# Kernel optimization log

Hardware: AMD Instinct MI355X
Metric: run time of the kernel (lower is better)

Reference implementation:

```python
import jax, jax.numpy as jnp
import numpy as np

N_NODES = 100000


def _gcn_conv(x, W, b, src, dst, n_nodes):
    # PyG GCNConv: h = x @ W; add self-loops; symmetric normalization
    # deg over destination (with self-loops), norm = d^-1/2[src] * d^-1/2[dst];
    # out[dst] += norm * h[src]; then + bias.
    h = x @ W  # [N, out_dim]
    loop = jnp.arange(n_nodes, dtype=src.dtype)
    s = jnp.concatenate([src, loop])
    d = jnp.concatenate([dst, loop])
    deg = jax.ops.segment_sum(jnp.ones_like(s, dtype=h.dtype), d, num_segments=n_nodes)
    dinv = jnp.where(deg > 0, jax.lax.rsqrt(deg), 0.0)
    norm = dinv[s] * dinv[d]  # [E+N]
    msg = h[s] * norm[:, None]  # gather + scale
    out = jax.ops.segment_sum(msg, d, num_segments=n_nodes)
    return out + b


def setup_inputs() -> dict:
    key = jax.random.key(0)
    k1, k2, k3, k4 = jax.random.split(key, 4)
    n, f, h, e = N_NODES, 128, 16, 3200000
    x = jax.random.normal(k1, (n, f), dtype=jnp.float32)
    edge_index = jax.random.randint(k2, (2, e), 0, n, dtype=jnp.int64)
    W1 = jax.random.normal(k3, (f, h), dtype=jnp.float32) * (1.0 / np.sqrt(f))
    b1 = jnp.zeros((h,), dtype=jnp.float32)
    W2 = jax.random.normal(k4, (h, h), dtype=jnp.float32) * (1.0 / np.sqrt(h))
    b2 = jnp.zeros((h,), dtype=jnp.float32)
    return {"x": x, "edge_index": edge_index, "W1": W1, "b1": b1, "W2": W2, "b2": b2}


def reference(x, edge_index, W1, b1, W2, b2):
    src, dst = edge_index[0], edge_index[1]
    h = _gcn_conv(x, W1, b1, src, dst, N_NODES)
    h = jax.nn.relu(h)
    out = _gcn_conv(h, W2, b2, src, dst, N_NODES)
    return out
```

## Files before the change

### kernel.cpp

```cpp
#include <hip/hip_runtime.h>

#define N_NODES 100000
#define F_IN 128
#define HD 16
#define NBKT 782
#define NPB 128
#define CHUNK 32768

__global__ __launch_bounds__(256) void k_bcnt(const int* __restrict__ dst, int* __restrict__ wgcnt,
                                              int E, int nwg) {
    __shared__ int hist[NBKT];
    const int t = threadIdx.x, wg = blockIdx.x;
    for (int b = t; b < NBKT; b += 256) hist[b] = 0;
    __syncthreads();
    const int e0 = wg * CHUNK;
    for (int it = 0; it < CHUNK / 1024; ++it) {
        int idx = e0 + it * 1024 + t * 4;
        if (idx + 3 < E) {
            int4 d = *(const int4*)(dst + idx);
            atomicAdd(&hist[d.x >> 7], 1);
            atomicAdd(&hist[d.y >> 7], 1);
            atomicAdd(&hist[d.z >> 7], 1);
            atomicAdd(&hist[d.w >> 7], 1);
        } else {
            int lim = min(idx + 4, E);
            for (int e = idx; e < lim; ++e) atomicAdd(&hist[dst[e] >> 7], 1);
        }
    }
    __syncthreads();
    for (int b = t; b < NBKT; b += 256) wgcnt[b * nwg + wg] = hist[b];
}

__global__ __launch_bounds__(128) void k_btot(const int* __restrict__ wgcnt, int* __restrict__ tot, int nwg) {
    __shared__ int s[128];
    const int b = blockIdx.x, t = threadIdx.x;
    s[t] = (t < nwg) ? wgcnt[b * nwg + t] : 0;
    __syncthreads();
    for (int off = 64; off > 0; off >>= 1) { if (t < off) s[t] += s[t + off]; __syncthreads(); }
    if (t == 0) tot[b] = s[0];
}

__global__ __launch_bounds__(1024) void k_escan(const int* __restrict__ tot, int* __restrict__ ebase) {
    __shared__ int s[1024];
    const int t = threadIdx.x;
    int v = (t < NBKT) ? tot[t] : 0;
    s[t] = v; __syncthreads();
    for (int off = 1; off < 1024; off <<= 1) {
        int x = (t >= off) ? s[t - off] : 0;
        __syncthreads();
        s[t] += x;
        __syncthreads();
    }
    if (t < NBKT) ebase[t] = s[t] - v;
    if (t == NBKT - 1) ebase[NBKT] = s[t];
}

__global__ __launch_bounds__(128) void k_bscan(const int* __restrict__ wgcnt, const int* __restrict__ ebase,
                                               int* __restrict__ base, int nwg) {
    __shared__ int s[128];
    const int b = blockIdx.x, t = threadIdx.x;
    int v = (t < nwg) ? wgcnt[b * nwg + t] : 0;
    s[t] = v; __syncthreads();
    for (int off = 1; off < 128; off <<= 1) {
        int x = (t >= off) ? s[t - off] : 0;
        __syncthreads();
        s[t] += x;
        __syncthreads();
    }
    if (t < nwg) base[b * nwg + t] = ebase[b] + s[t] - v;
}

__global__ __launch_bounds__(256) void k_bscatter(const int* __restrict__ src, const int* __restrict__ dst,
                                                  const int* __restrict__ base, unsigned* __restrict__ srt,
                                                  int E, int nwg) {
    __shared__ int cur[NBKT];
    const int t = threadIdx.x, wg = blockIdx.x;
    for (int b = t; b < NBKT; b += 256) cur[b] = base[b * nwg + wg];
    __syncthreads();
    const int e0 = wg * CHUNK;
    for (int it = 0; it < CHUNK / 1024; ++it) {
        int idx = e0 + it * 1024 + t * 4;
        if (idx + 3 < E) {
            int4 s4 = *(const int4*)(src + idx);
            int4 d4 = *(const int4*)(dst + idx);
            int p;
            p = atomicAdd(&cur[d4.x >> 7], 1); srt[p] = ((unsigned)s4.x << 7) | (unsigned)(d4.x & 127);
            p = atomicAdd(&cur[d4.y >> 7], 1); srt[p] = ((unsigned)s4.y << 7) | (unsigned)(d4.y & 127);
            p = atomicAdd(&cur[d4.z >> 7], 1); srt[p] = ((unsigned)s4.z << 7) | (unsigned)(d4.z & 127);
            p = atomicAdd(&cur[d4.w >> 7], 1); srt[p] = ((unsigned)s4.w << 7) | (unsigned)(d4.w & 127);
        } else {
            int lim = min(idx + 4, E);
            for (int e = idx; e < lim; ++e) {
                int p = atomicAdd(&cur[dst[e] >> 7], 1);
                srt[p] = ((unsigned)src[e] << 7) | (unsigned)(dst[e] & 127);
            }
        }
    }
}

__global__ __launch_bounds__(256) void k_bsort(const unsigned* __restrict__ srt,
                                               const int* __restrict__ ebase,
                                               int* __restrict__ srt2,
                                               int* __restrict__ rs,
                                               float* __restrict__ dinv) {
    __shared__ int cnt_s[NPB];
    __shared__ int sc[NPB];
    __shared__ int cur_s[NPB];
    const int t = threadIdx.x, b = blockIdx.x;
    const int beg = ebase[b], end = ebase[b + 1];

    if (t < NPB) cnt_s[t] = 0;
    __syncthreads();
    for (int i = beg + t; i < end; i += 256) atomicAdd(&cnt_s[srt[i] & 127], 1);
    __syncthreads();

    if (t < NPB) sc[t] = cnt_s[t];
    __syncthreads();
    for (int off = 1; off < NPB; off <<= 1) {
        int v = (t < NPB && t >= off) ? sc[t - off] : 0;
        __syncthreads();
        if (t < NPB) sc[t] += v;
        __syncthreads();
    }
    if (t < NPB) {
        int start = beg + sc[t] - cnt_s[t];
        cur_s[t] = start;
        int node = b * NPB + t;
        if (node <= N_NODES) rs[node] = start;
        if (node < N_NODES) dinv[node] = rsqrtf((float)(cnt_s[t] + 1));
    }
    __syncthreads();
    for (int i = beg + t; i < end; i += 256) {
        unsigned p = srt[i];
        int pos = atomicAdd(&cur_s[p & 127], 1);
        srt2[pos] = (int)(p >> 7);
    }
}

__global__ __launch_bounds__(256) void k_h1(
        const float* __restrict__ x, const float* __restrict__ W1,
        const float* __restrict__ dinv, float* __restrict__ hs) {
    __shared__ float ws[F_IN * HD];
    __shared__ float xs[16][F_IN + 1];
    const int t = threadIdx.x;
    const int node0 = blockIdx.x * 16;

    for (int i = t; i < F_IN * HD; i += 256) ws[i] = W1[i];
    for (int i = t; i < 16 * F_IN; i += 256) {
        int r = i >> 7, c = i & 127;
        int n = node0 + r;
        xs[r][c] = (n < N_NODES) ? x[n * F_IN + c] : 0.0f;
    }
    __syncthreads();

    const int row = t >> 4, col = t & 15;
    const int node = node0 + row;
    float acc = 0.0f;
#pragma unroll 8
    for (int k = 0; k < F_IN; ++k)
        acc += xs[row][k] * ws[k * HD + col];

    if (node < N_NODES) hs[node * HD + col] = acc * dinv[node];
}

__global__ __launch_bounds__(256) void k_h2(
        const float* __restrict__ out1, const float* __restrict__ W2,
        const float* __restrict__ dinv, float* __restrict__ hs) {
    __shared__ float ws[HD * HD];
    __shared__ float as[16][HD + 1];
    const int t = threadIdx.x;
    const int node0 = blockIdx.x * 16;

    if (t < HD * HD) ws[t] = W2[t];
    {
        int n = node0 + (t >> 4);
        float v = (n < N_NODES) ? out1[node0 * HD + t] : 0.0f;
        as[t >> 4][t & 15] = fmaxf(v, 0.0f);
    }
    __syncthreads();

    const int row = t >> 4, col = t & 15;
    const int node = node0 + row;
    float acc = 0.0f;
#pragma unroll
    for (int k = 0; k < HD; ++k)
        acc += as[row][k] * ws[k * HD + col];

    if (node < N_NODES) hs[node * HD + col] = acc * dinv[node];
}

__global__ __launch_bounds__(256) void k_agg(
        const int* __restrict__ srt2, const int* __restrict__ rs,
        const float* __restrict__ dinv, const float* __restrict__ hs,
        const float* __restrict__ bias, float* __restrict__ out) {
    const int node = blockIdx.x * 4 + (threadIdx.x >> 6);
    if (node >= N_NODES) return;
    const int lane = threadIdx.x & 63;
    const int slot = lane >> 2;
    const int c4 = lane & 3;

    const int beg = rs[node];
    const int n   = rs[node + 1] - beg;
    const float4* __restrict__ h4 = (const float4*)hs;

    float4 a = make_float4(0.0f, 0.0f, 0.0f, 0.0f);
    for (int i = slot; i < n; i += 16) {
        int s = srt2[beg + i];
        float4 v = h4[s * 4 + c4];
        a.x += v.x; a.y += v.y; a.z += v.z; a.w += v.w;
    }
#pragma unroll
    for (int m = 4; m <= 32; m <<= 1) {
        a.x += __shfl_xor(a.x, m);
        a.y += __shfl_xor(a.y, m);
        a.z += __shfl_xor(a.z, m);
        a.w += __shfl_xor(a.w, m);
    }
    if (slot == 0) {
        float4 hv = h4[node * 4 + c4];
        float4 bb = ((const float4*)bias)[c4];
        float dd = dinv[node];
        float4 o;
        o.x = dd * (a.x + hv.x) + bb.x;
        o.y = dd * (a.y + hv.y) + bb.y;
        o.z = dd * (a.z + hv.z) + bb.z;
        o.w = dd * (a.w + hv.w) + bb.w;
        ((float4*)out)[node * 4 + c4] = o;
    }
}

extern "C" void kernel_launch(void* const* d_in, const int* in_sizes, int n_in,
                              void* d_out, int out_size, void* d_ws, size_t ws_size,
                              hipStream_t stream) {
    const float* x   = (const float*)d_in[0];
    const int*   ei  = (const int*)d_in[1];
    const float* W1  = (const float*)d_in[2];
    const float* b1  = (const float*)d_in[3];
    const float* W2  = (const float*)d_in[4];
    const float* b2  = (const float*)d_in[5];
    float* out = (float*)d_out;

    const int E = in_sizes[1] / 2;
    const int* src = ei;
    const int* dst = ei + E;
    const int nwg = (E + CHUNK - 1) / CHUNK;

    char* wsb = (char*)d_ws;
    int*      wgcnt = (int*)(wsb + 0x0000000);
    int*      base  = (int*)(wsb + 0x0060000);
    int*      tot   = (int*)(wsb + 0x00C0000);
    int*      ebase = (int*)(wsb + 0x00C2000);
    float*    dinv  = (float*)(wsb + 0x00D0000);
    int*      rs    = (int*)(wsb + 0x0140000);
    unsigned* srt   = (unsigned*)(wsb + 0x0200000);
    float*    hs    = (float*)(wsb + 0x0200000);
    float*    out1  = (float*)(wsb + 0x0900000);
    int*      srt2  = (int*)(wsb + 0x1000000);

    const int tileBlocks = (N_NODES + 15) / 16;
    const int aggBlocks  = (N_NODES + 3) / 4;

    k_bcnt<<<nwg, 256, 0, stream>>>(dst, wgcnt, E, nwg);
    k_btot<<<NBKT, 128, 0, stream>>>(wgcnt, tot, nwg);
    k_escan<<<1, 1024, 0, stream>>>(tot, ebase);
    k_bscan<<<NBKT, 128, 0, stream>>>(wgcnt, ebase, base, nwg);
    k_bscatter<<<nwg, 256, 0, stream>>>(src, dst, base, srt, E, nwg);
    k_bsort<<<NBKT, 256, 0, stream>>>(srt, ebase, srt2, rs, dinv);

    k_h1<<<tileBlocks, 256, 0, stream>>>(x, W1, dinv, hs);
    k_agg<<<aggBlocks, 256, 0, stream>>>(srt2, rs, dinv, hs, b1, out1);

    k_h2<<<tileBlocks, 256, 0, stream>>>(out1, W2, dinv, hs);
    k_agg<<<aggBlocks, 256, 0, stream>>>(srt2, rs, dinv, hs, b2, out);
}
```

Measured before the change: 305.7 us.

## Store node features in fp16 for aggregation gathers and shrink sort chunks

```diff
diff --git a/kernel.cpp b/kernel.cpp
--- a/kernel.cpp
+++ b/kernel.cpp
@@ -1,21 +1,25 @@
 #include <hip/hip_runtime.h>
+#include <hip/hip_fp16.h>
 
 #define N_NODES 100000
 #define F_IN 128
 #define HD 16
 #define NBKT 782
 #define NPB 128
-#define CHUNK 32768
-
-__global__ __launch_bounds__(256) void k_bcnt(const int* __restrict__ dst, int* __restrict__ wgcnt,
-                                              int E, int nwg) {
+#define CHUNK 8192
+#define BTHREADS 512
+
+typedef __attribute__((ext_vector_type(4))) _Float16 half4;
+
+__global__ __launch_bounds__(BTHREADS) void k_bcnt(const int* __restrict__ dst, int* __restrict__ wgcnt,
+                                                   int E, int nwg) {
     __shared__ int hist[NBKT];
     const int t = threadIdx.x, wg = blockIdx.x;
-    for (int b = t; b < NBKT; b += 256) hist[b] = 0;
+    for (int b = t; b < NBKT; b += BTHREADS) hist[b] = 0;
     __syncthreads();
     const int e0 = wg * CHUNK;
-    for (int it = 0; it < CHUNK / 1024; ++it) {
-        int idx = e0 + it * 1024 + t * 4;
+    for (int it = 0; it < CHUNK / (BTHREADS * 4); ++it) {
+        int idx = e0 + it * (BTHREADS * 4) + t * 4;
         if (idx + 3 < E) {
             int4 d = *(const int4*)(dst + idx);
             atomicAdd(&hist[d.x >> 7], 1);
@@ -28,15 +32,15 @@
         }
     }
     __syncthreads();
-    for (int b = t; b < NBKT; b += 256) wgcnt[b * nwg + wg] = hist[b];
-}
-
-__global__ __launch_bounds__(128) void k_btot(const int* __restrict__ wgcnt, int* __restrict__ tot, int nwg) {
-    __shared__ int s[128];
+    for (int b = t; b < NBKT; b += BTHREADS) wgcnt[b * nwg + wg] = hist[b];
+}
+
+__global__ __launch_bounds__(512) void k_btot(const int* __restrict__ wgcnt, int* __restrict__ tot, int nwg) {
+    __shared__ int s[512];
     const int b = blockIdx.x, t = threadIdx.x;
     s[t] = (t < nwg) ? wgcnt[b * nwg + t] : 0;
     __syncthreads();
-    for (int off = 64; off > 0; off >>= 1) { if (t < off) s[t] += s[t + off]; __syncthreads(); }
+    for (int off = 256; off > 0; off >>= 1) { if (t < off) s[t] += s[t + off]; __syncthreads(); }
     if (t == 0) tot[b] = s[0];
 }
 
@@ -55,13 +59,13 @@
     if (t == NBKT - 1) ebase[NBKT] = s[t];
 }
 
-__global__ __launch_bounds__(128) void k_bscan(const int* __restrict__ wgcnt, const int* __restrict__ ebase,
+__global__ __launch_bounds__(512) void k_bscan(const int* __restrict__ wgcnt, const int* __restrict__ ebase,
                                                int* __restrict__ base, int nwg) {
-    __shared__ int s[128];
+    __shared__ int s[512];
     const int b = blockIdx.x, t = threadIdx.x;
     int v = (t < nwg) ? wgcnt[b * nwg + t] : 0;
     s[t] = v; __syncthreads();
-    for (int off = 1; off < 128; off <<= 1) {
+    for (int off = 1; off < 512; off <<= 1) {
         int x = (t >= off) ? s[t - off] : 0;
         __syncthreads();
         s[t] += x;
@@ -70,16 +74,16 @@
     if (t < nwg) base[b * nwg + t] = ebase[b] + s[t] - v;
 }
 
-__global__ __launch_bounds__(256) void k_bscatter(const int* __restrict__ src, const int* __restrict__ dst,
-                                                  const int* __restrict__ base, unsigned* __restrict__ srt,
-                                                  int E, int nwg) {
+__global__ __launch_bounds__(BTHREADS) void k_bscatter(const int* __restrict__ src, const int* __restrict__ dst,
+                                                       const int* __restrict__ base, unsigned* __restrict__ srt,
+                                                       int E, int nwg) {
     __shared__ int cur[NBKT];
     const int t = threadIdx.x, wg = blockIdx.x;
-    for (int b = t; b < NBKT; b += 256) cur[b] = base[b * nwg + wg];
+    for (int b = t; b < NBKT; b += BTHREADS) cur[b] = base[b * nwg + wg];
     __syncthreads();
     const int e0 = wg * CHUNK;
-    for (int it = 0; it < CHUNK / 1024; ++it) {
-        int idx = e0 + it * 1024 + t * 4;
+    for (int it = 0; it < CHUNK / (BTHREADS * 4); ++it) {
+        int idx = e0 + it * (BTHREADS * 4) + t * 4;
         if (idx + 3 < E) {
             int4 s4 = *(const int4*)(src + idx);
             int4 d4 = *(const int4*)(dst + idx);
@@ -139,7 +143,7 @@
 
 __global__ __launch_bounds__(256) void k_h1(
         const float* __restrict__ x, const float* __restrict__ W1,
-        const float* __restrict__ dinv, float* __restrict__ hs) {
+        const float* __restrict__ dinv, _Float16* __restrict__ hs) {
     __shared__ float ws[F_IN * HD];
     __shared__ float xs[16][F_IN + 1];
     const int t = threadIdx.x;
@@ -160,12 +164,12 @@
     for (int k = 0; k < F_IN; ++k)
         acc += xs[row][k] * ws[k * HD + col];
 
-    if (node < N_NODES) hs[node * HD + col] = acc * dinv[node];
+    if (node < N_NODES) hs[node * HD + col] = (_Float16)(acc * dinv[node]);
 }
 
 __global__ __launch_bounds__(256) void k_h2(
         const float* __restrict__ out1, const float* __restrict__ W2,
-        const float* __restrict__ dinv, float* __restrict__ hs) {
+        const float* __restrict__ dinv, _Float16* __restrict__ hs) {
     __shared__ float ws[HD * HD];
     __shared__ float as[16][HD + 1];
     const int t = threadIdx.x;
@@ -186,12 +190,12 @@
     for (int k = 0; k < HD; ++k)
         acc += as[row][k] * ws[k * HD + col];
 
-    if (node < N_NODES) hs[node * HD + col] = acc * dinv[node];
+    if (node < N_NODES) hs[node * HD + col] = (_Float16)(acc * dinv[node]);
 }
 
 __global__ __launch_bounds__(256) void k_agg(
         const int* __restrict__ srt2, const int* __restrict__ rs,
-        const float* __restrict__ dinv, const float* __restrict__ hs,
+        const float* __restrict__ dinv, const _Float16* __restrict__ hs,
         const float* __restrict__ bias, float* __restrict__ out) {
     const int node = blockIdx.x * 4 + (threadIdx.x >> 6);
     if (node >= N_NODES) return;
@@ -201,30 +205,30 @@
 
     const int beg = rs[node];
     const int n   = rs[node + 1] - beg;
-    const float4* __restrict__ h4 = (const float4*)hs;
-
-    float4 a = make_float4(0.0f, 0.0f, 0.0f, 0.0f);
+    const half4* __restrict__ h4 = (const half4*)hs;
+
+    float ax = 0.0f, ay = 0.0f, az = 0.0f, aw = 0.0f;
     for (int i = slot; i < n; i += 16) {
         int s = srt2[beg + i];
-        float4 v = h4[s * 4 + c4];
-        a.x += v.x; a.y += v.y; a.z += v.z; a.w += v.w;
+        half4 v = h4[s * 4 + c4];
+        ax += (float)v.x; ay += (float)v.y; az += (float)v.z; aw += (float)v.w;
     }
 #pragma unroll
     for (int m = 4; m <= 32; m <<= 1) {
-        a.x += __shfl_xor(a.x, m);
-        a.y += __shfl_xor(a.y, m);
-        a.z += __shfl_xor(a.z, m);
-        a.w += __shfl_xor(a.w, m);
+        ax += __shfl_xor(ax, m);
+        ay += __shfl_xor(ay, m);
+        az += __shfl_xor(az, m);
+        aw += __shfl_xor(aw, m);
     }
     if (slot == 0) {
-        float4 hv = h4[node * 4 + c4];
+        half4 hv = h4[node * 4 + c4];
         float4 bb = ((const float4*)bias)[c4];
         float dd = dinv[node];
         float4 o;
-        o.x = dd * (a.x + hv.x) + bb.x;
-        o.y = dd * (a.y + hv.y) + bb.y;
-        o.z = dd * (a.z + hv.z) + bb.z;
-        o.w = dd * (a.w + hv.w) + bb.w;
+        o.x = dd * (ax + (float)hv.x) + bb.x;
+        o.y = dd * (ay + (float)hv.y) + bb.y;
+        o.z = dd * (az + (float)hv.z) + bb.z;
+        o.w = dd * (aw + (float)hv.w) + bb.w;
         ((float4*)out)[node * 4 + c4] = o;
     }
 }
@@ -246,25 +250,25 @@
     const int nwg = (E + CHUNK - 1) / CHUNK;
 
     char* wsb = (char*)d_ws;
-    int*      wgcnt = (int*)(wsb + 0x0000000);
-    int*      base  = (int*)(wsb + 0x0060000);
-    int*      tot   = (int*)(wsb + 0x00C0000);
-    int*      ebase = (int*)(wsb + 0x00C2000);
-    float*    dinv  = (float*)(wsb + 0x00D0000);
-    int*      rs    = (int*)(wsb + 0x0140000);
-    unsigned* srt   = (unsigned*)(wsb + 0x0200000);
-    float*    hs    = (float*)(wsb + 0x0200000);
-    float*    out1  = (float*)(wsb + 0x0900000);
-    int*      srt2  = (int*)(wsb + 0x1000000);
+    int*      tot   = (int*)(wsb + 0x0000000);
+    int*      ebase = (int*)(wsb + 0x0001000);
+    float*    dinv  = (float*)(wsb + 0x0002000);
+    int*      rs    = (int*)(wsb + 0x0070000);
+    unsigned* srt   = (unsigned*)(wsb + 0x0100000);
+    _Float16* hs    = (_Float16*)(wsb + 0x0100000);
+    float*    out1  = (float*)(wsb + 0x0500000);
+    int*      srt2  = (int*)(wsb + 0x0D40000);
+    int*      wgcnt = (int*)(wsb + 0x0D40000);
+    int*      base  = (int*)(wsb + 0x0F00000);
 
     const int tileBlocks = (N_NODES + 15) / 16;
     const int aggBlocks  = (N_NODES + 3) / 4;
 
-    k_bcnt<<<nwg, 256, 0, stream>>>(dst, wgcnt, E, nwg);
-    k_btot<<<NBKT, 128, 0, stream>>>(wgcnt, tot, nwg);
+    k_bcnt<<<nwg, BTHREADS, 0, stream>>>(dst, wgcnt, E, nwg);
+    k_btot<<<NBKT, 512, 0, stream>>>(wgcnt, tot, nwg);
     k_escan<<<1, 1024, 0, stream>>>(tot, ebase);
-    k_bscan<<<NBKT, 128, 0, stream>>>(wgcnt, ebase, base, nwg);
-    k_bscatter<<<nwg, 256, 0, stream>>>(src, dst, base, srt, E, nwg);
+    k_bscan<<<NBKT, 512, 0, stream>>>(wgcnt, ebase, base, nwg);
+    k_bscatter<<<nwg, BTHREADS, 0, stream>>>(src, dst, base, srt, E, nwg);
     k_bsort<<<NBKT, 256, 0, stream>>>(srt, ebase, srt2, rs, dinv);
 
     k_h1<<<tileBlocks, 256, 0, stream>>>(x, W1, dinv, hs);
```

Result: faster. 283.9 us (-7.1%).
